# Kernel optimization log

Measured on AMD Instinct MI355X. Metric: run time of the kernel, lower is better.

Reference implementation:

```python
import jax, jax.numpy as jnp
import numpy as np

EPS = 1e-5

def _ln(x, g, b):
    mu = jnp.mean(x, axis=-1, keepdims=True)
    var = jnp.mean(jnp.square(x - mu), axis=-1, keepdims=True)
    return (x - mu) * jax.lax.rsqrt(var + EPS) * g + b

def _lrelu(x):
    return jnp.where(x >= 0, x, 0.1 * x)  # LeakyReLU(0.1)

def _layer(x, w, b, g, be, act):
    # PointLinearLayer: Linear -> LayerNorm -> (optional) LeakyReLU(0.1)
    y = _ln(jnp.matmul(x, w) + b, g, be)
    return _lrelu(y) if act else y

def setup_inputs():
    key = jax.random.key(0)
    ks = jax.random.split(key, 16)
    B, Ns, Nd, K, Cin, Cout, PE, M = 1, 10000, 40000, 16, 128, 128, 32, 16
    w = lambda k, i, o: jax.random.normal(k, (i, o), jnp.float32) * 0.02
    z = lambda n: jnp.zeros((n,), jnp.float32)
    o = lambda n: jnp.ones((n,), jnp.float32)
    return {
        "sparse_xyz": jax.random.normal(ks[0], (B, Ns, 3), jnp.float32),
        "sparse_feats": jax.random.normal(ks[1], (B, Ns, Cin), jnp.float32),
        "nei_inds": jax.random.randint(ks[2], (B, Nd, K), 0, Ns),
        "sparse_xyz_norm": jax.random.normal(ks[3], (B, Ns, 3), jnp.float32),
        "dense_xyz": jax.random.normal(ks[4], (B, Nd, 3), jnp.float32),
        "dense_xyz_norm": jax.random.normal(ks[5], (B, Nd, 3), jnp.float32),
        "dense_feats": jax.random.normal(ks[6], (B, Nd, Cout), jnp.float32),
        # pe_convs WeightNet(3 -> 32, hidden=[32]): L0 3->32 LN+act, L1 32->32 LN
        "pe_w0": w(ks[7], 3, PE), "pe_b0": z(PE), "pe_g0": o(PE), "pe_be0": z(PE),
        "pe_w1": w(ks[8], PE, PE), "pe_b1": z(PE), "pe_g1": o(PE), "pe_be1": z(PE),
        # main WeightNet(3 -> 16, hidden=[16,16]): L0,L1 LN+act, L2 LN
        "wn_w0": w(ks[9], 3, M), "wn_b0": z(M), "wn_g0": o(M), "wn_be0": z(M),
        "wn_w1": w(ks[10], M, M), "wn_b1": z(M), "wn_g1": o(M), "wn_be1": z(M),
        "wn_w2": w(ks[11], M, M), "wn_b2": z(M), "wn_g2": o(M), "wn_be2": z(M),
        # final PointLinearLayer: (Cin+PE)*M -> Cout with LN + LeakyReLU(0.1)
        "lin_w": w(ks[12], (Cin + PE) * M, Cout), "lin_b": z(Cout),
        "lin_g": o(Cout), "lin_be": z(Cout),
    }

def reference(sparse_xyz, sparse_feats, nei_inds, sparse_xyz_norm, dense_xyz,
              dense_xyz_norm, dense_feats,
              pe_w0, pe_b0, pe_g0, pe_be0, pe_w1, pe_b1, pe_g1, pe_be1,
              wn_w0, wn_b0, wn_g0, wn_be0, wn_w1, wn_b1, wn_g1, wn_be1,
              wn_w2, wn_b2, wn_g2, wn_be2, lin_w, lin_b, lin_g, lin_be):
    gather = jax.vmap(lambda t, i: t[i])  # per-batch kNN gather
    loc = gather(sparse_xyz, nei_inds) - dense_xyz[:, :, None, :]   # B,Nd,K,3 relative coords (weightNetInput, USE_VI=False)
    g_feat = gather(sparse_feats, nei_inds)                          # B,Nd,K,Cin
    # positional-encoding WeightNet on relative coords (USE_PE)
    pe = _layer(loc, pe_w0, pe_b0, pe_g0, pe_be0, True)
    pe = _layer(pe, pe_w1, pe_b1, pe_g1, pe_be1, False)              # B,Nd,K,32
    feat = jnp.concatenate([g_feat, pe], axis=-1)                    # B,Nd,K,Cin+32
    # main WeightNet generates per-neighbor mixing weights
    wts = _layer(loc, wn_w0, wn_b0, wn_g0, wn_be0, True)
    wts = _layer(wts, wn_w1, wn_b1, wn_g1, wn_be1, True)
    wts = _layer(wts, wn_w2, wn_b2, wn_g2, wn_be2, False)            # B,Nd,K,16
    B, Nd = nei_inds.shape[:2]
    # matmul(feat^T, wts) over K, flatten channel x mid dims (C-major, matches torch .view)
    out = jnp.einsum('bnkc,bnkm->bncm', feat, wts).reshape(B, Nd, -1)
    out = _layer(out, lin_w, lin_b, lin_g, lin_be, True)             # B,Nd,Cout
    return out + dense_feats                                         # shortcut dense features
```

## Files before the change

### kernel.cpp

```cpp
#include <hip/hip_runtime.h>

#define NPB  16
#define KNN  16
#define CIN  128
#define CF   160
#define MM   16
#define PEC  32
#define COUT 128
#define KDIM 2560
#define LEPS 1e-5f

typedef __bf16 bf16x8 __attribute__((ext_vector_type(8)));
typedef float  f32x4  __attribute__((ext_vector_type(4)));
union U16x8 { uint4 u4; bf16x8 b; unsigned short us[8]; };

#define SW_PE_W0   0
#define SW_PE_B0   96
#define SW_PE_G0   128
#define SW_PE_BE0  160
#define SW_PE_W1   192
#define SW_PE_B1   1216
#define SW_PE_G1   1248
#define SW_PE_BE1  1280
#define SW_WN_W0   1312
#define SW_WN_B0   1360
#define SW_WN_G0   1376
#define SW_WN_BE0  1392
#define SW_WN_W1   1408
#define SW_WN_B1   1664
#define SW_WN_G1   1680
#define SW_WN_BE1  1696
#define SW_WN_W2   1712
#define SW_WN_B2   1968
#define SW_WN_G2   1984
#define SW_WN_BE2  2000
#define SW_TOTAL   2016

__device__ __forceinline__ float bf2f(unsigned short b){
  union { unsigned int u; float f; } x; x.u = ((unsigned int)b) << 16; return x.f;
}
__device__ __forceinline__ unsigned short f2bf(float f){
  union { float f; unsigned int u; } x; x.f = f;
  unsigned int r = (x.u + 0x7fffu + ((x.u >> 16) & 1u)) >> 16;
  return (unsigned short)r;
}
__device__ __forceinline__ unsigned short f2b(float f){
  union { __bf16 h; unsigned short u; } v; v.h = (__bf16)f; return v.u;
}
__device__ __forceinline__ float rsum16(float v){
  v += __shfl_xor(v, 8, 16);
  v += __shfl_xor(v, 4, 16);
  v += __shfl_xor(v, 2, 16);
  v += __shfl_xor(v, 1, 16);
  return v;
}
__device__ __forceinline__ float rsum8(float v){
  v += __shfl_xor(v, 4, 8);
  v += __shfl_xor(v, 2, 8);
  v += __shfl_xor(v, 1, 8);
  return v;
}
__device__ __forceinline__ float rsum32(float v){
  v += __shfl_xor(v, 16, 32);
  v += __shfl_xor(v, 8, 32);
  v += __shfl_xor(v, 4, 32);
  v += __shfl_xor(v, 2, 32);
  v += __shfl_xor(v, 1, 32);
  return v;
}
__device__ __forceinline__ float lrelu(float v){ return v >= 0.f ? v : 0.1f * v; }

template<int N>
__device__ __forceinline__ void ln_inlane(float* v, const float* g, const float* be, bool act){
  float mu = 0.f;
#pragma unroll
  for (int i = 0; i < N; ++i) mu += v[i];
  mu *= (1.f / N);
  float var = 0.f;
#pragma unroll
  for (int i = 0; i < N; ++i) { float d = v[i] - mu; var += d * d; }
  const float rs = rsqrtf(var * (1.f / N) + LEPS);
#pragma unroll
  for (int i = 0; i < N; ++i) {
    float y = (v[i] - mu) * rs * g[i] + be[i];
    v[i] = act ? lrelu(y) : y;
  }
}

__global__ __launch_bounds__(256)
void pct_feats_bf16(const float* __restrict__ sf, unsigned short* __restrict__ o, const int n4)
{
  const int i = blockIdx.x * 256 + threadIdx.x;
  if (i >= n4) return;
  const float4 v = ((const float4*)sf)[i];
  union { unsigned short us[4]; uint2 u; } r;
  r.us[0] = f2b(v.x); r.us[1] = f2b(v.y); r.us[2] = f2b(v.z); r.us[3] = f2b(v.w);
  ((uint2*)o)[i] = r.u;
}

__global__ __launch_bounds__(256)
void pct_pack_w(const float* __restrict__ lin_w, unsigned short* __restrict__ wpack)
{
  const int u    = blockIdx.x * 256 + threadIdx.x;
  const int lane = u & 63;
  const int tt   = (u >> 6) & 7;
  const int s    = u >> 9;
  const int ipb  = s * 32 + ((lane >> 4) * 8);
  const int nn   = tt * 16 + (lane & 15);
  unsigned short v[8];
#pragma unroll
  for (int j = 0; j < 8; ++j) {
    const int ip  = ipb + j;
    const int r   = ip & 3;
    const int ctl = (ip >> 2) & 1;
    const int qq  = (ip >> 3) & 3;
    const int c16 = (ip >> 5) & 15;
    const int P   = ip >> 9;
    const int c   = P * 32 + ctl * 16 + c16;
    const int m   = qq * 4 + r;
    v[j] = f2bf(lin_w[(long)(c * MM + m) * COUT + nn]);
  }
  *(uint4*)(wpack + (long)u * 8) = *(uint4*)v;
}

__global__ __launch_bounds__(256)
void pct_einsum_mfma(
    const float* __restrict__ sparse_xyz,
    const int* __restrict__ nei_inds,
    const float* __restrict__ dense_xyz,
    const unsigned short* __restrict__ sfb16,
    const float* __restrict__ pe_w0, const float* __restrict__ pe_b0,
    const float* __restrict__ pe_g0, const float* __restrict__ pe_be0,
    const float* __restrict__ pe_w1, const float* __restrict__ pe_b1,
    const float* __restrict__ pe_g1, const float* __restrict__ pe_be1,
    const float* __restrict__ wn_w0, const float* __restrict__ wn_b0,
    const float* __restrict__ wn_g0, const float* __restrict__ wn_be0,
    const float* __restrict__ wn_w1, const float* __restrict__ wn_b1,
    const float* __restrict__ wn_g1, const float* __restrict__ wn_be1,
    const float* __restrict__ wn_w2, const float* __restrict__ wn_b2,
    const float* __restrict__ wn_g2, const float* __restrict__ wn_be2,
    unsigned short* __restrict__ apack)
{
  __shared__ __align__(16) float zeroblk[128];
  __shared__ __align__(16) unsigned short wtsf[16 * 256];
  __shared__ __align__(16) unsigned short pef[16 * 512];
  __shared__ __align__(16) union SU {
    float sw[SW_TOTAL];
    char  stage[4 * 2 * 4096];
  } su;
  float* sw = su.sw;

  const int t     = threadIdx.x;
  const int nbase = blockIdx.x * NPB;

  if (t < 128) zeroblk[t] = 0.f;
  for (int i = t; i < 96;   i += 256) sw[SW_PE_W0 + i] = pe_w0[i];
  for (int i = t; i < 32;   i += 256) {
    sw[SW_PE_B0 + i] = pe_b0[i];  sw[SW_PE_G0 + i] = pe_g0[i];  sw[SW_PE_BE0 + i] = pe_be0[i];
    sw[SW_PE_B1 + i] = pe_b1[i];  sw[SW_PE_G1 + i] = pe_g1[i];  sw[SW_PE_BE1 + i] = pe_be1[i];
  }
  for (int i = t; i < 1024; i += 256) sw[SW_PE_W1 + i] = pe_w1[i];
  for (int i = t; i < 48;   i += 256) sw[SW_WN_W0 + i] = wn_w0[i];
  for (int i = t; i < 16;   i += 256) {
    sw[SW_WN_B0 + i] = wn_b0[i];  sw[SW_WN_G0 + i] = wn_g0[i];  sw[SW_WN_BE0 + i] = wn_be0[i];
    sw[SW_WN_B1 + i] = wn_b1[i];  sw[SW_WN_G1 + i] = wn_g1[i];  sw[SW_WN_BE1 + i] = wn_be1[i];
    sw[SW_WN_B2 + i] = wn_b2[i];  sw[SW_WN_G2 + i] = wn_g2[i];  sw[SW_WN_BE2 + i] = wn_be2[i];
  }
  for (int i = t; i < 256;  i += 256) { sw[SW_WN_W1 + i] = wn_w1[i]; sw[SW_WN_W2 + i] = wn_w2[i]; }
  __syncthreads();

  {
    const int p  = t >> 4;
    const int kk = t & 15;
    const int n  = nbase + p;
    const int idx = nei_inds[n * KNN + kk];
    const float x0 = sparse_xyz[idx*3+0] - dense_xyz[n*3+0];
    const float x1 = sparse_xyz[idx*3+1] - dense_xyz[n*3+1];
    const float x2 = sparse_xyz[idx*3+2] - dense_xyz[n*3+2];

    float h[32];
#pragma unroll
    for (int c = 0; c < 32; ++c)
      h[c] = x0*sw[SW_PE_W0+c] + x1*sw[SW_PE_W0+32+c] + x2*sw[SW_PE_W0+64+c] + sw[SW_PE_B0+c];
    ln_inlane<32>(h, &sw[SW_PE_G0], &sw[SW_PE_BE0], true);

    float z[32];
#pragma unroll
    for (int c = 0; c < 32; ++c) z[c] = sw[SW_PE_B1 + c];
#pragma unroll 4
    for (int j = 0; j < 32; ++j) {
      const float hj = h[j];
#pragma unroll
      for (int c = 0; c < 32; ++c) z[c] += hj * sw[SW_PE_W1 + j*32 + c];
    }
    ln_inlane<32>(z, &sw[SW_PE_G1], &sw[SW_PE_BE1], false);
    {
      union { unsigned short us[32]; uint4 u4[4]; } zb;
#pragma unroll
      for (int c = 0; c < 32; ++c) zb.us[c] = f2b(z[c]);
      unsigned short* pp_ = pef + p*512 + kk*32;
#pragma unroll
      for (int j = 0; j < 4; ++j) *(uint4*)(pp_ + j*8) = zb.u4[j];
    }

    float w[16];
#pragma unroll
    for (int m = 0; m < 16; ++m)
      w[m] = x0*sw[SW_WN_W0+m] + x1*sw[SW_WN_W0+16+m] + x2*sw[SW_WN_W0+32+m] + sw[SW_WN_B0+m];
    ln_inlane<16>(w, &sw[SW_WN_G0], &sw[SW_WN_BE0], true);

    float z2[16];
#pragma unroll
    for (int m = 0; m < 16; ++m) z2[m] = sw[SW_WN_B1 + m];
#pragma unroll 4
    for (int j = 0; j < 16; ++j) {
      const float wj = w[j];
#pragma unroll
      for (int m = 0; m < 16; ++m) z2[m] += wj * sw[SW_WN_W1 + j*16 + m];
    }
    ln_inlane<16>(z2, &sw[SW_WN_G1], &sw[SW_WN_BE1], true);

#pragma unroll
    for (int m = 0; m < 16; ++m) w[m] = sw[SW_WN_B2 + m];
#pragma unroll 4
    for (int j = 0; j < 16; ++j) {
      const float wj = z2[j];
#pragma unroll
      for (int m = 0; m < 16; ++m) w[m] += wj * sw[SW_WN_W2 + j*16 + m];
    }
    ln_inlane<16>(w, &sw[SW_WN_G2], &sw[SW_WN_BE2], false);
    {
      unsigned short* wf = wtsf + p*256 + ((kk >> 3) << 7) + (kk & 7);
#pragma unroll
      for (int m = 0; m < 16; ++m) wf[m*8] = f2b(w[m]);
    }
  }
  __syncthreads();

  const int lane = t & 63;
  const int wave = t >> 6;
  const int q    = lane >> 4;
  const int mq   = lane & 15;
  char* stw = su.stage + wave * 8192;

  int idxall[4][4];
#pragma unroll
  for (int i = 0; i < 4; ++i)
#pragma unroll
    for (int t4 = 0; t4 < 4; ++t4)
      idxall[i][t4] = nei_inds[(nbase + wave*4 + i) * KNN + t4*4 + q];

#pragma unroll
  for (int t4 = 0; t4 < 4; ++t4)
    __builtin_amdgcn_global_load_lds(
        (const void*)(sfb16 + (size_t)idxall[0][t4] * CIN + mq * 8),
        (void*)(stw + t4 * 1024), 16, 0, 0);

  f32x4 accs[10];
#pragma unroll
  for (int i = 0; i < 4; ++i) {
    const int p = wave * 4 + i;
    const size_t n = (size_t)(nbase + p);

    if (i < 3) {
#pragma unroll
      for (int t4 = 0; t4 < 4; ++t4)
        __builtin_amdgcn_global_load_lds(
            (const void*)(sfb16 + (size_t)idxall[i+1][t4] * CIN + mq * 8),
            (void*)(stw + ((i+1) & 1) * 4096 + t4 * 1024), 16, 0, 0);
      asm volatile("s_waitcnt vmcnt(4)" ::: "memory");
    } else {
      asm volatile("s_waitcnt vmcnt(0)" ::: "memory");
    }
    __builtin_amdgcn_sched_barrier(0);

    U16x8 af;
    {
      const unsigned short* ap_ = (lane < 32)
          ? wtsf + p * 256 + lane * 8
          : (const unsigned short*)zeroblk + (lane - 32) * 8;
      af.u4 = *(const uint4*)ap_;
    }
#pragma unroll
    for (int ct = 0; ct < 10; ++ct) accs[ct] = (f32x4){0.f, 0.f, 0.f, 0.f};

    const unsigned short* sb = (const unsigned short*)(stw + (i & 1) * 4096)
                               + (q & 1) * 1024 + mq;
#pragma unroll
    for (int ct = 0; ct < 8; ++ct) {
      U16x8 bf_;
#pragma unroll
      for (int j = 0; j < 8; ++j) bf_.us[j] = sb[j * CIN + ct * 16];
      accs[ct] = __builtin_amdgcn_mfma_f32_16x16x32_bf16(af.b, bf_.b, accs[ct], 0, 0, 0);
    }
    const unsigned short* pb = pef + p * 512 + (q & 1) * 256 + mq;
#pragma unroll
    for (int ct = 0; ct < 2; ++ct) {
      U16x8 bf_;
#pragma unroll
      for (int j = 0; j < 8; ++j) bf_.us[j] = pb[j * 32 + ct * 16];
      accs[8 + ct] = __builtin_amdgcn_mfma_f32_16x16x32_bf16(af.b, bf_.b, accs[8 + ct], 0, 0, 0);
    }

    unsigned short* ap = apack + n * KDIM + mq * 32 + q * 8;
#pragma unroll
    for (int P = 0; P < 5; ++P) {
      union { unsigned short us[8]; uint4 u4; } o;
#pragma unroll
      for (int r = 0; r < 4; ++r) {
        o.us[r]     = f2b(accs[2*P    ][r]);
        o.us[4 + r] = f2b(accs[2*P + 1][r]);
      }
      *(uint4*)(ap + P * 512) = o.u4;
    }
  }
}

__global__ __launch_bounds__(256)
void pct_gemm32(
    const unsigned short* __restrict__ apack,
    const unsigned short* __restrict__ wpack,
    const float* __restrict__ lin_b, const float* __restrict__ lin_g,
    const float* __restrict__ lin_be, const float* __restrict__ dense_feats,
    float* __restrict__ out)
{
  __shared__ float out_s[32][132];

  const int t    = threadIdx.x;
  const int lane = t & 63;
  const int wave = t >> 6;
  const int n0   = blockIdx.x * 32;

  const unsigned short* arow0 = apack + (long)(n0 + (lane & 15)) * KDIM + ((lane >> 4) * 8);
  const unsigned short* arow1 = arow0 + (long)16 * KDIM;
  const unsigned short* wp0   = wpack + ((long)(wave*2) * 64 + lane) * 8;

  f32x4 acc00 = {0.f,0.f,0.f,0.f}, acc01 = {0.f,0.f,0.f,0.f};
  f32x4 acc10 = {0.f,0.f,0.f,0.f}, acc11 = {0.f,0.f,0.f,0.f};

  U16x8 a0[4], a1[4], b0[4], b1[4];
#pragma unroll
  for (int d = 0; d < 4; ++d) {
    a0[d].u4 = *(const uint4*)(arow0 + d*32);
    a1[d].u4 = *(const uint4*)(arow1 + d*32);
    b0[d].u4 = *(const uint4*)(wp0 + (long)d*4096);
    b1[d].u4 = *(const uint4*)(wp0 + (long)d*4096 + 512);
  }

#pragma unroll 4
  for (int s = 0; s < 80; ++s) {
    const int d = s & 3;
    acc00 = __builtin_amdgcn_mfma_f32_16x16x32_bf16(a0[d].b, b0[d].b, acc00, 0, 0, 0);
    acc01 = __builtin_amdgcn_mfma_f32_16x16x32_bf16(a0[d].b, b1[d].b, acc01, 0, 0, 0);
    acc10 = __builtin_amdgcn_mfma_f32_16x16x32_bf16(a1[d].b, b0[d].b, acc10, 0, 0, 0);
    acc11 = __builtin_amdgcn_mfma_f32_16x16x32_bf16(a1[d].b, b1[d].b, acc11, 0, 0, 0);
    if (s + 4 < 80) {
      a0[d].u4 = *(const uint4*)(arow0 + (s+4)*32);
      a1[d].u4 = *(const uint4*)(arow1 + (s+4)*32);
      b0[d].u4 = *(const uint4*)(wp0 + (long)(s+4)*4096);
      b1[d].u4 = *(const uint4*)(wp0 + (long)(s+4)*4096 + 512);
    }
  }

  {
    const int quad = lane >> 4;
    const int colb = wave*32 + (lane & 15);
#pragma unroll
    for (int r = 0; r < 4; ++r) {
      out_s[     quad*4 + r][colb     ] = acc00[r];
      out_s[     quad*4 + r][colb + 16] = acc01[r];
      out_s[16 + quad*4 + r][colb     ] = acc10[r];
      out_s[16 + quad*4 + r][colb + 16] = acc11[r];
    }
  }
  __syncthreads();

  {
    const int p  = t >> 3;
    const int l8 = t & 7;
    const int n  = n0 + p;
    float v[16];
#pragma unroll
    for (int i = 0; i < 4; ++i) {
      const int cb = (i*8 + l8) * 4;
      const float4 r  = *(const float4*)(&out_s[p][cb]);
      const float4 bb = *(const float4*)(lin_b + cb);
      v[i*4+0] = r.x + bb.x; v[i*4+1] = r.y + bb.y;
      v[i*4+2] = r.z + bb.z; v[i*4+3] = r.w + bb.w;
    }
    float sum = 0.f;
#pragma unroll
    for (int i = 0; i < 16; ++i) sum += v[i];
    const float mu = rsum8(sum) * (1.f/128.f);
    float qs = 0.f;
#pragma unroll
    for (int i = 0; i < 16; ++i) { float d = v[i] - mu; qs += d*d; }
    const float rs = rsqrtf(rsum8(qs) * (1.f/128.f) + LEPS);
#pragma unroll
    for (int i = 0; i < 4; ++i) {
      const int cb = (i*8 + l8) * 4;
      const float4 g  = *(const float4*)(lin_g  + cb);
      const float4 be = *(const float4*)(lin_be + cb);
      const float4 df = *(const float4*)(dense_feats + (long)n*COUT + cb);
      float4 y;
      y.x = lrelu((v[i*4+0]-mu)*rs*g.x + be.x) + df.x;
      y.y = lrelu((v[i*4+1]-mu)*rs*g.y + be.y) + df.y;
      y.z = lrelu((v[i*4+2]-mu)*rs*g.z + be.z) + df.z;
      y.w = lrelu((v[i*4+3]-mu)*rs*g.w + be.w) + df.w;
      *(float4*)(out + (long)n*COUT + cb) = y;
    }
  }
}

__global__ __launch_bounds__(256)
void pct_fused(
    const float* __restrict__ sparse_xyz,
    const float* __restrict__ sparse_feats,
    const int* __restrict__ nei_inds,
    const float* __restrict__ dense_xyz,
    const float* __restrict__ dense_feats,
    const float* __restrict__ pe_w0, const float* __restrict__ pe_b0,
    const float* __restrict__ pe_g0, const float* __restrict__ pe_be0,
    const float* __restrict__ pe_w1, const float* __restrict__ pe_b1,
    const float* __restrict__ pe_g1, const float* __restrict__ pe_be1,
    const float* __restrict__ wn_w0, const float* __restrict__ wn_b0,
    const float* __restrict__ wn_g0, const float* __restrict__ wn_be0,
    const float* __restrict__ wn_w1, const float* __restrict__ wn_b1,
    const float* __restrict__ wn_g1, const float* __restrict__ wn_be1,
    const float* __restrict__ wn_w2, const float* __restrict__ wn_b2,
    const float* __restrict__ wn_g2, const float* __restrict__ wn_be2,
    const float* __restrict__ lin_w, const float* __restrict__ lin_b,
    const float* __restrict__ lin_g, const float* __restrict__ lin_be,
    float* __restrict__ out)
{
  __shared__ __align__(16) unsigned short feat_s[KNN][CF];
  __shared__ float wts_s[KNN][MM];
  __shared__ float loc_s[KNN][3];
  __shared__ int   nei_s[KNN];
  __shared__ __align__(16) unsigned short out_tile[CF*MM][8];

  const int t  = threadIdx.x;
  const int n0 = blockIdx.x * 8;
  const int k  = t >> 4;
  const int l  = t & 15;

#pragma unroll 1
  for (int p = 0; p < 8; ++p) {
    const int n = n0 + p;
    if (t < KNN) {
      int idx = nei_inds[n*KNN + t];
      nei_s[t] = idx;
      loc_s[t][0] = sparse_xyz[idx*3+0] - dense_xyz[n*3+0];
      loc_s[t][1] = sparse_xyz[idx*3+1] - dense_xyz[n*3+1];
      loc_s[t][2] = sparse_xyz[idx*3+2] - dense_xyz[n*3+2];
    }
    __syncthreads();
    {
      const int gk = t >> 4;
      const int c8 = (t & 15) * 8;
      const float* src = sparse_feats + (long)nei_s[gk]*CIN + c8;
      const float4 va = *(const float4*)(src);
      const float4 vb = *(const float4*)(src + 4);
      unsigned short* dst = &feat_s[gk][c8];
      dst[0] = f2bf(va.x); dst[1] = f2bf(va.y); dst[2] = f2bf(va.z); dst[3] = f2bf(va.w);
      dst[4] = f2bf(vb.x); dst[5] = f2bf(vb.y); dst[6] = f2bf(vb.z); dst[7] = f2bf(vb.w);
    }
    const float x0 = loc_s[k][0], x1 = loc_s[k][1], x2 = loc_s[k][2];
    const int c0 = l, c1 = l + 16;
    float ha = x0*pe_w0[0*PEC+c0] + x1*pe_w0[1*PEC+c0] + x2*pe_w0[2*PEC+c0] + pe_b0[c0];
    float hb = x0*pe_w0[0*PEC+c1] + x1*pe_w0[1*PEC+c1] + x2*pe_w0[2*PEC+c1] + pe_b0[c1];
    {
      float mu = rsum16(ha + hb) * (1.f/32.f);
      float da = ha - mu, db = hb - mu;
      float q  = rsum16(da*da + db*db);
      float rs = rsqrtf(q*(1.f/32.f) + LEPS);
      ha = lrelu(da*rs*pe_g0[c0] + pe_be0[c0]);
      hb = lrelu(db*rs*pe_g0[c1] + pe_be0[c1]);
    }
    float za = pe_b1[c0], zb = pe_b1[c1];
#pragma unroll
    for (int j = 0; j < 16; ++j) {
      float va = __shfl(ha, j, 16);
      float vb = __shfl(hb, j, 16);
      za += va * pe_w1[j*PEC + c0] + vb * pe_w1[(j+16)*PEC + c0];
      zb += va * pe_w1[j*PEC + c1] + vb * pe_w1[(j+16)*PEC + c1];
    }
    {
      float mu = rsum16(za + zb) * (1.f/32.f);
      float da = za - mu, db = zb - mu;
      float q  = rsum16(da*da + db*db);
      float rs = rsqrtf(q*(1.f/32.f) + LEPS);
      feat_s[k][CIN + c0] = f2bf(da*rs*pe_g1[c0] + pe_be1[c0]);
      feat_s[k][CIN + c1] = f2bf(db*rs*pe_g1[c1] + pe_be1[c1]);
    }
    float w0v = x0*wn_w0[0*MM+l] + x1*wn_w0[1*MM+l] + x2*wn_w0[2*MM+l] + wn_b0[l];
    {
      float mu = rsum16(w0v) * (1.f/16.f);
      float d  = w0v - mu;
      float rs = rsqrtf(rsum16(d*d)*(1.f/16.f) + LEPS);
      w0v = lrelu(d*rs*wn_g0[l] + wn_be0[l]);
    }
    float w1v = wn_b1[l];
#pragma unroll
    for (int j = 0; j < 16; ++j)
      w1v += __shfl(w0v, j, 16) * wn_w1[j*MM + l];
    {
      float mu = rsum16(w1v) * (1.f/16.f);
      float d  = w1v - mu;
      float rs = rsqrtf(rsum16(d*d)*(1.f/16.f) + LEPS);
      w1v = lrelu(d*rs*wn_g1[l] + wn_be1[l]);
    }
    float w2v = wn_b2[l];
#pragma unroll
    for (int j = 0; j < 16; ++j)
      w2v += __shfl(w1v, j, 16) * wn_w2[j*MM + l];
    {
      float mu = rsum16(w2v) * (1.f/16.f);
      float d  = w2v - mu;
      float rs = rsqrtf(rsum16(d*d)*(1.f/16.f) + LEPS);
      w2v = d*rs*wn_g2[l] + wn_be2[l];
    }
    wts_s[k][l] = w2v;
    __syncthreads();
    {
      const int m = t & 15;
      const int g = t >> 4;
      float wv[KNN];
#pragma unroll
      for (int kk = 0; kk < KNN; ++kk) wv[kk] = wts_s[kk][m];
#pragma unroll
      for (int j = 0; j < 10; ++j) {
        const int c = g*10 + j;
        float acc = 0.f;
#pragma unroll
        for (int kk = 0; kk < KNN; ++kk)
          acc += bf2f(feat_s[kk][c]) * wv[kk];
        out_tile[c*MM + m][p] = f2bf(acc);
      }
    }
    __syncthreads();
  }
  {
    const int h  = t >> 6;
    const int o0 = (t & 63) * 2;
    float acc0[8], acc1[8];
#pragma unroll
    for (int p = 0; p < 8; ++p) { acc0[p] = 0.f; acc1[p] = 0.f; }
    const int i0 = h * 640;
    for (int i = i0; i < i0 + 640; ++i) {
      const float2 wv = *(const float2*)(lin_w + (long)i*COUT + o0);
      const float wa = wv.x;
      const float wc = wv.y;
      const uint4 r = *(const uint4*)(&out_tile[i][0]);
      const float f0 = bf2f((unsigned short)(r.x & 0xffffu));
      const float f1 = bf2f((unsigned short)(r.x >> 16));
      const float g2 = bf2f((unsigned short)(r.y & 0xffffu));
      const float g3 = bf2f((unsigned short)(r.y >> 16));
      const float g4 = bf2f((unsigned short)(r.z & 0xffffu));
      const float g5 = bf2f((unsigned short)(r.z >> 16));
      const float g6 = bf2f((unsigned short)(r.w & 0xffffu));
      const float g7 = bf2f((unsigned short)(r.w >> 16));
      acc0[0] += f0*wa; acc1[0] += f0*wc;
      acc0[1] += f1*wa; acc1[1] += f1*wc;
      acc0[2] += g2*wa; acc1[2] += g2*wc;
      acc0[3] += g3*wa; acc1[3] += g3*wc;
      acc0[4] += g4*wa; acc1[4] += g4*wc;
      acc0[5] += g5*wa; acc1[5] += g5*wc;
      acc0[6] += g6*wa; acc1[6] += g6*wc;
      acc0[7] += g7*wa; acc1[7] += g7*wc;
    }
    __syncthreads();
    float* red = (float*)&out_tile[0][0];
#pragma unroll
    for (int p = 0; p < 8; ++p) {
      red[((h*8 + p) << 7) + o0    ] = acc0[p];
      red[((h*8 + p) << 7) + o0 + 1] = acc1[p];
    }
    __syncthreads();
    const int p2 = t >> 5, l2 = t & 31;
    const int n  = n0 + p2;
    float v[4];
#pragma unroll
    for (int j = 0; j < 4; ++j) {
      const int o = l2 + (j << 5);
      float sv = red[((0*8 + p2) << 7) + o] + red[((1*8 + p2) << 7) + o]
               + red[((2*8 + p2) << 7) + o] + red[((3*8 + p2) << 7) + o];
      v[j] = sv + lin_b[o];
    }
    float mu = rsum32(v[0] + v[1] + v[2] + v[3]) * (1.f/128.f);
    float q = 0.f;
#pragma unroll
    for (int j = 0; j < 4; ++j) { float d = v[j] - mu; q += d*d; }
    float rs = rsqrtf(rsum32(q) * (1.f/128.f) + LEPS);
#pragma unroll
    for (int j = 0; j < 4; ++j) {
      const int o = l2 + (j << 5);
      float y = (v[j] - mu) * rs * lin_g[o] + lin_be[o];
      y = lrelu(y);
      y += dense_feats[n*COUT + o];
      out[n*COUT + o] = y;
    }
  }
}

extern "C" void kernel_launch(void* const* d_in, const int* in_sizes, int n_in,
                              void* d_out, int out_size, void* d_ws, size_t ws_size,
                              hipStream_t stream) {
  const int Nd = in_sizes[2] / KNN;
  const int Ns = in_sizes[1] / CIN;
  const size_t a_bytes = (size_t)Nd * KDIM * 2;
  const size_t w_bytes = (size_t)KDIM * COUT * 2;
  const size_t f_bytes = (size_t)Ns * CIN * 2;
  const bool use_split = (ws_size >= a_bytes + w_bytes + f_bytes)
                         && (Nd % 32 == 0) && ((Ns * CIN) % 4 == 0);

  if (use_split) {
    unsigned short* apack = (unsigned short*)d_ws;
    unsigned short* wpack = (unsigned short*)((char*)d_ws + a_bytes);
    unsigned short* sfb16 = (unsigned short*)((char*)d_ws + a_bytes + w_bytes);

    pct_pack_w<<<dim3((KDIM/32)*8*64/256), dim3(256), 0, stream>>>(
      (const float*)d_in[27], wpack);

    const int n4 = Ns * CIN / 4;
    pct_feats_bf16<<<dim3((n4 + 255)/256), dim3(256), 0, stream>>>(
      (const float*)d_in[1], sfb16, n4);

    pct_einsum_mfma<<<dim3(Nd / NPB), dim3(256), 0, stream>>>(
      (const float*)d_in[0],  (const int*)d_in[2],  (const float*)d_in[4],
      sfb16,
      (const float*)d_in[7],  (const float*)d_in[8],  (const float*)d_in[9],  (const float*)d_in[10],
      (const float*)d_in[11], (const float*)d_in[12], (const float*)d_in[13], (const float*)d_in[14],
      (const float*)d_in[15], (const float*)d_in[16], (const float*)d_in[17], (const float*)d_in[18],
      (const float*)d_in[19], (const float*)d_in[20], (const float*)d_in[21], (const float*)d_in[22],
      (const float*)d_in[23], (const float*)d_in[24], (const float*)d_in[25], (const float*)d_in[26],
      apack);

    pct_gemm32<<<dim3(Nd / 32), dim3(256), 0, stream>>>(
      apack, wpack,
      (const float*)d_in[28], (const float*)d_in[29], (const float*)d_in[30],
      (const float*)d_in[6], (float*)d_out);
  } else {
    pct_fused<<<dim3(Nd / 8), dim3(256), 0, stream>>>(
      (const float*)d_in[0],  (const float*)d_in[1],  (const int*)d_in[2],
      (const float*)d_in[4],  (const float*)d_in[6],
      (const float*)d_in[7],  (const float*)d_in[8],  (const float*)d_in[9],  (const float*)d_in[10],
      (const float*)d_in[11], (const float*)d_in[12], (const float*)d_in[13], (const float*)d_in[14],
      (const float*)d_in[15], (const float*)d_in[16], (const float*)d_in[17], (const float*)d_in[18],
      (const float*)d_in[19], (const float*)d_in[20], (const float*)d_in[21], (const float*)d_in[22],
      (const float*)d_in[23], (const float*)d_in[24], (const float*)d_in[25], (const float*)d_in[26],
      (const float*)d_in[27], (const float*)d_in[28], (const float*)d_in[29], (const float*)d_in[30],
      (float*)d_out);
  }
}
```

Before: 346.6 us.

## Merge prep kernels, relax einsum vmcnt waits, peel and schedule gemm loop

```diff
diff --git a/kernel.cpp b/kernel.cpp
--- a/kernel.cpp
+++ b/kernel.cpp
@@ -88,39 +88,40 @@
 }
 
 __global__ __launch_bounds__(256)
-void pct_feats_bf16(const float* __restrict__ sf, unsigned short* __restrict__ o, const int n4)
+void pct_prep(const float* __restrict__ lin_w, unsigned short* __restrict__ wpack,
+              const float* __restrict__ sf, unsigned short* __restrict__ sfb16,
+              const int n4)
 {
-  const int i = blockIdx.x * 256 + threadIdx.x;
-  if (i >= n4) return;
-  const float4 v = ((const float4*)sf)[i];
-  union { unsigned short us[4]; uint2 u; } r;
-  r.us[0] = f2b(v.x); r.us[1] = f2b(v.y); r.us[2] = f2b(v.z); r.us[3] = f2b(v.w);
-  ((uint2*)o)[i] = r.u;
-}
-
-__global__ __launch_bounds__(256)
-void pct_pack_w(const float* __restrict__ lin_w, unsigned short* __restrict__ wpack)
-{
-  const int u    = blockIdx.x * 256 + threadIdx.x;
-  const int lane = u & 63;
-  const int tt   = (u >> 6) & 7;
-  const int s    = u >> 9;
-  const int ipb  = s * 32 + ((lane >> 4) * 8);
-  const int nn   = tt * 16 + (lane & 15);
-  unsigned short v[8];
-#pragma unroll
-  for (int j = 0; j < 8; ++j) {
-    const int ip  = ipb + j;
-    const int r   = ip & 3;
-    const int ctl = (ip >> 2) & 1;
-    const int qq  = (ip >> 3) & 3;
-    const int c16 = (ip >> 5) & 15;
-    const int P   = ip >> 9;
-    const int c   = P * 32 + ctl * 16 + c16;
-    const int m   = qq * 4 + r;
-    v[j] = f2bf(lin_w[(long)(c * MM + m) * COUT + nn]);
-  }
-  *(uint4*)(wpack + (long)u * 8) = *(uint4*)v;
+  const int bid = blockIdx.x;
+  if (bid < 160) {
+    const int u    = bid * 256 + threadIdx.x;
+    const int lane = u & 63;
+    const int tt   = (u >> 6) & 7;
+    const int s    = u >> 9;
+    const int ipb  = s * 32 + ((lane >> 4) * 8);
+    const int nn   = tt * 16 + (lane & 15);
+    unsigned short v[8];
+#pragma unroll
+    for (int j = 0; j < 8; ++j) {
+      const int ip  = ipb + j;
+      const int r   = ip & 3;
+      const int ctl = (ip >> 2) & 1;
+      const int qq  = (ip >> 3) & 3;
+      const int c16 = (ip >> 5) & 15;
+      const int P   = ip >> 9;
+      const int c   = P * 32 + ctl * 16 + c16;
+      const int m   = qq * 4 + r;
+      v[j] = f2bf(lin_w[(long)(c * MM + m) * COUT + nn]);
+    }
+    *(uint4*)(wpack + (long)u * 8) = *(uint4*)v;
+  } else {
+    const int i = (bid - 160) * 256 + threadIdx.x;
+    if (i >= n4) return;
+    const float4 v = ((const float4*)sf)[i];
+    union { unsigned short us[4]; uint2 u; } r;
+    r.us[0] = f2b(v.x); r.us[1] = f2b(v.y); r.us[2] = f2b(v.z); r.us[3] = f2b(v.w);
+    ((uint2*)sfb16)[i] = r.u;
+  }
 }
 
 __global__ __launch_bounds__(256)
@@ -268,10 +269,11 @@
         __builtin_amdgcn_global_load_lds(
             (const void*)(sfb16 + (size_t)idxall[i+1][t4] * CIN + mq * 8),
             (void*)(stw + ((i+1) & 1) * 4096 + t4 * 1024), 16, 0, 0);
-      asm volatile("s_waitcnt vmcnt(4)" ::: "memory");
-    } else {
-      asm volatile("s_waitcnt vmcnt(0)" ::: "memory");
-    }
+    }
+    if (i == 0)      asm volatile("s_waitcnt vmcnt(4)" ::: "memory");
+    else if (i == 1) asm volatile("s_waitcnt vmcnt(9)" ::: "memory");
+    else if (i == 2) asm volatile("s_waitcnt vmcnt(9)" ::: "memory");
+    else             asm volatile("s_waitcnt vmcnt(5)" ::: "memory");
     __builtin_amdgcn_sched_barrier(0);
 
     U16x8 af;
@@ -316,7 +318,7 @@
   }
 }
 
-__global__ __launch_bounds__(256)
+__global__ __launch_bounds__(256, 4)
 void pct_gemm32(
     const unsigned short* __restrict__ apack,
     const unsigned short* __restrict__ wpack,
@@ -348,19 +350,29 @@
   }
 
 #pragma unroll 4
-  for (int s = 0; s < 80; ++s) {
+  for (int s = 0; s < 76; ++s) {
     const int d = s & 3;
+    __builtin_amdgcn_sched_barrier(0);
     acc00 = __builtin_amdgcn_mfma_f32_16x16x32_bf16(a0[d].b, b0[d].b, acc00, 0, 0, 0);
     acc01 = __builtin_amdgcn_mfma_f32_16x16x32_bf16(a0[d].b, b1[d].b, acc01, 0, 0, 0);
     acc10 = __builtin_amdgcn_mfma_f32_16x16x32_bf16(a1[d].b, b0[d].b, acc10, 0, 0, 0);
     acc11 = __builtin_amdgcn_mfma_f32_16x16x32_bf16(a1[d].b, b1[d].b, acc11, 0, 0, 0);
-    if (s + 4 < 80) {
-      a0[d].u4 = *(const uint4*)(arow0 + (s+4)*32);
-      a1[d].u4 = *(const uint4*)(arow1 + (s+4)*32);
-      b0[d].u4 = *(const uint4*)(wp0 + (long)(s+4)*4096);
-      b1[d].u4 = *(const uint4*)(wp0 + (long)(s+4)*4096 + 512);
-    }
-  }
+    __builtin_amdgcn_sched_barrier(0);
+    a0[d].u4 = *(const uint4*)(arow0 + (s+4)*32);
+    a1[d].u4 = *(const uint4*)(arow1 + (s+4)*32);
+    b0[d].u4 = *(const uint4*)(wp0 + (long)(s+4)*4096);
+    b1[d].u4 = *(const uint4*)(wp0 + (long)(s+4)*4096 + 512);
+  }
+#pragma unroll
+  for (int s = 76; s < 80; ++s) {
+    const int d = s & 3;
+    __builtin_amdgcn_sched_barrier(0);
+    acc00 = __builtin_amdgcn_mfma_f32_16x16x32_bf16(a0[d].b, b0[d].b, acc00, 0, 0, 0);
+    acc01 = __builtin_amdgcn_mfma_f32_16x16x32_bf16(a0[d].b, b1[d].b, acc01, 0, 0, 0);
+    acc10 = __builtin_amdgcn_mfma_f32_16x16x32_bf16(a1[d].b, b0[d].b, acc10, 0, 0, 0);
+    acc11 = __builtin_amdgcn_mfma_f32_16x16x32_bf16(a1[d].b, b1[d].b, acc11, 0, 0, 0);
+  }
+  __builtin_amdgcn_sched_barrier(0);
 
   {
     const int quad = lane >> 4;
@@ -619,12 +631,9 @@
     unsigned short* wpack = (unsigned short*)((char*)d_ws + a_bytes);
     unsigned short* sfb16 = (unsigned short*)((char*)d_ws + a_bytes + w_bytes);
 
-    pct_pack_w<<<dim3((KDIM/32)*8*64/256), dim3(256), 0, stream>>>(
-      (const float*)d_in[27], wpack);
-
     const int n4 = Ns * CIN / 4;
-    pct_feats_bf16<<<dim3((n4 + 255)/256), dim3(256), 0, stream>>>(
-      (const float*)d_in[1], sfb16, n4);
+    pct_prep<<<dim3(160 + (n4 + 255)/256), dim3(256), 0, stream>>>(
+      (const float*)d_in[27], wpack, (const float*)d_in[1], sfb16, n4);
 
     pct_einsum_mfma<<<dim3(Nd / NPB), dim3(256), 0, stream>>>(
       (const float*)d_in[0],  (const int*)d_in[2],  (const float*)d_in[4],
```

Result: no change. 341.2 us (-1.6%).
